# Kernel optimization log

Measured on AMD Instinct MI355X. Metric: run time of the kernel, lower is better.

Reference implementation:

```python
import jax, jax.numpy as jnp
import numpy as np

MARGIN = 0.3
EPS = 1e-12


def setup_inputs() -> dict:
    key = jax.random.key(0)
    k1, k2, k3 = jax.random.split(key, 3)
    B, D = 8192, 1024
    features = jax.random.normal(k1, (B, D), dtype=jnp.float32)
    labels = jax.random.randint(k2, (B,), 0, 100, dtype=jnp.int64)
    domain_labels = jax.random.randint(k3, (B,), 0, 2, dtype=jnp.int64)
    return {"features": features, "labels": labels, "domain_labels": domain_labels}


def reference(features, labels, domain_labels):
    # L2-normalize rows (F.normalize: x / max(||x||, eps))
    norm = jnp.maximum(jnp.linalg.norm(features, axis=1, keepdims=True), EPS)
    f = features / norm

    herb = domain_labels == 0   # [B] anchors
    field = domain_labels == 1  # [B] candidates

    sq = jnp.sum(f * f, axis=1)                                   # [B]
    d2 = sq[:, None] + sq[None, :] - 2.0 * jnp.einsum('id,jd->ij', f, f)
    d = jnp.sqrt(jnp.maximum(d2, 0.0))                            # [B, B]

    same = labels[:, None] == labels[None, :]                     # [B, B]
    pair = herb[:, None] & field[None, :]
    pos_mask = pair & same
    neg_mask = pair & ~same

    INF = jnp.float32(jnp.inf)
    pos_min = jnp.min(jnp.where(pos_mask, d, INF), axis=1)        # [B]
    neg_min = jnp.min(jnp.where(neg_mask, d, INF), axis=1)        # [B]

    valid = herb & jnp.any(pos_mask, axis=1) & jnp.any(neg_mask, axis=1)
    # Substitute 0 for invalid rows BEFORE subtracting to avoid inf - inf.
    pos_s = jnp.where(valid, pos_min, 0.0)
    neg_s = jnp.where(valid, neg_min, 0.0)
    tl = jnp.maximum(pos_s - neg_s + MARGIN, 0.0)                 # [B]

    loss_sum = jnp.sum(jnp.where(valid, tl, 0.0))
    count = jnp.sum(valid.astype(jnp.float32))
    return jnp.where(count > 0, loss_sum / jnp.maximum(count, 1.0), 0.0)
```

## Files before the change

### kernel.cpp

```cpp
#include <hip/hip_runtime.h>


#define B_ROWS 8192
#define DIM    1024

typedef __bf16 bf16x8 __attribute__((ext_vector_type(8)));
typedef float  f32x4  __attribute__((ext_vector_type(4)));

__device__ __forceinline__ unsigned short f2bf_rne(float x) {
    unsigned u = __float_as_uint(x);
    unsigned r = (u + 0x7FFFu + ((u >> 16) & 1u)) >> 16;
    return (unsigned short)r;
}
__device__ __forceinline__ float bf2f(unsigned short h) {
    return __uint_as_float(((unsigned)h) << 16);
}

__device__ __forceinline__ void async_copy16(const void* g, void* l) {
    __builtin_amdgcn_global_load_lds(
        (const __attribute__((address_space(1))) unsigned int*)g,
        (__attribute__((address_space(3))) unsigned int*)l,
        16, 0, 0);
}

__global__ __launch_bounds__(256) void compute_slots(
    const int* __restrict__ dom, int* __restrict__ slotOf,
    unsigned* __restrict__ cnt, float* __restrict__ accum)
{
    __shared__ int cnts[256];
    __shared__ int base[257];
    const int t = threadIdx.x;

    if (t == 0) {
        cnt[1] = 0u;
        accum[0] = 0.0f;
        accum[1] = 0.0f;
    }

    unsigned mask = 0u; int c = 0;
    #pragma unroll
    for (int i = 0; i < 32; ++i) {
        const int isA = (dom[t + 256 * i] == 0) ? 1 : 0;
        mask |= ((unsigned)isA) << i;
        c += isA;
    }
    cnts[t] = c;
    __syncthreads();
    if (t < 64) {
        const int c0 = cnts[4 * t + 0], c1 = cnts[4 * t + 1];
        const int c2 = cnts[4 * t + 2], c3 = cnts[4 * t + 3];
        const int s4 = c0 + c1 + c2 + c3;
        int sc = s4;
        #pragma unroll
        for (int d = 1; d < 64; d <<= 1) {
            const int o = __shfl_up(sc, d);
            if (t >= d) sc += o;
        }
        const int b = sc - s4;
        base[4 * t + 0] = b;
        base[4 * t + 1] = b + c0;
        base[4 * t + 2] = b + c0 + c1;
        base[4 * t + 3] = b + c0 + c1 + c2;
        if (t == 63) { base[256] = sc; cnt[0] = (unsigned)sc; }
    }
    __syncthreads();
    int aB = base[t];
    int fI = t * 32 - base[t];
    #pragma unroll
    for (int i = 0; i < 32; ++i) {
        const int isA = (mask >> i) & 1;
        slotOf[t + 256 * i] = isA ? aB : (8191 - fI);
        aB += isA;
        fI += 1 - isA;
    }
}

__global__ __launch_bounds__(256) void normalize_rows(
    const float* __restrict__ feat, const int* __restrict__ labels,
    int* slotOf , unsigned* __restrict__ negmin,
    unsigned short* __restrict__ G, int* __restrict__ labG,
    float* __restrict__ sqG)
{
    const int wv = threadIdx.x >> 6, lane = threadIdx.x & 63;
    const int row = blockIdx.x * 4 + wv;

    const float4* src = (const float4*)(feat + (size_t)row * DIM);
    float4 v[4];
    float ss = 0.0f;
    #pragma unroll
    for (int j = 0; j < 4; ++j) {
        v[j] = src[j * 64 + lane];
        ss += v[j].x * v[j].x + v[j].y * v[j].y + v[j].z * v[j].z + v[j].w * v[j].w;
    }
    #pragma unroll
    for (int s = 32; s > 0; s >>= 1) ss += __shfl_xor(ss, s);
    const float inv = 1.0f / fmaxf(sqrtf(ss), 1e-12f);

    const int slot = slotOf[row];
    if (lane == 0) {
        ((unsigned*)slotOf)[row] = 0xFFFFFFFFu;
        negmin[row] = 0xFFFFFFFFu;
    }
    unsigned short ub[16];
    float ss2 = 0.0f;
    #pragma unroll
    for (int j = 0; j < 4; ++j) {
        const float f0 = v[j].x * inv, f1 = v[j].y * inv,
                    f2 = v[j].z * inv, f3 = v[j].w * inv;
        ub[j * 4 + 0] = f2bf_rne(f0); ub[j * 4 + 1] = f2bf_rne(f1);
        ub[j * 4 + 2] = f2bf_rne(f2); ub[j * 4 + 3] = f2bf_rne(f3);
        #pragma unroll
        for (int q = 0; q < 4; ++q) {
            const float fr = bf2f(ub[j * 4 + q]);
            ss2 += fr * fr;
        }
    }
    #pragma unroll
    for (int s = 32; s > 0; s >>= 1) ss2 += __shfl_xor(ss2, s);
    if (lane == 0) {
        sqG[slot]  = ss2;
        labG[slot] = labels[row];
    }
    char* Gb = (char*)G;
    char* rowBase = Gb + (size_t)(slot >> 7) * 262144 + (size_t)(slot & 127) * 64
                       + (lane & 7) * 8;
    const int kc0 = lane >> 3;
    #pragma unroll
    for (int j = 0; j < 4; ++j) {
        ushort4 pk;
        pk.x = ub[j * 4 + 0]; pk.y = ub[j * 4 + 1];
        pk.z = ub[j * 4 + 2]; pk.w = ub[j * 4 + 3];
        *(ushort4*)(rowBase + (size_t)(j * 8 + kc0) * 8192) = pk;
    }
}

__global__ __launch_bounds__(256) void tile_mindist(
    const unsigned short* __restrict__ G, const int* __restrict__ labG,
    const float* __restrict__ sqG, const unsigned* __restrict__ cnt,
    unsigned* __restrict__ posmin, unsigned* __restrict__ negmin)
{
    const int nA = (int)cnt[0];
    const int nF = B_ROWS - nA;
    const int nTA = (nA + 127) >> 7;
    const int nTF = (nF + 127) >> 7;

    __shared__ __align__(16) unsigned short S[2][2][128 * 32];

    const int t = threadIdx.x;
    const int lane = t & 63, w = t >> 6;
    const int wm = w >> 1, wn = w & 1;
    const int l15 = lane & 15, quad = lane >> 4;

    const int ch0 = 2 * w;

    const int rdA  = (wm * 64 + l15) * 32 + quad * 8;
    const int rdF0 = ((1 - wn) * 64 + 15 - l15) * 32 + quad * 8;

    const char* Gb = (const char*)G;

    const int xcd = blockIdx.x & 7;
    const int bx  = xcd & 1;
    const int by  = xcd >> 1;
    const int qa = nTA >> 1, ra = nTA & 1;
    const int sa = qa + ((bx < ra) ? 1 : 0);
    const int xa = bx * qa + ((bx < ra) ? bx : ra);
    const int qf = nTF >> 2, rf = nTF & 3;
    const int sf = qf + ((by < rf) ? 1 : 0);
    const int ya = by * qf + ((by < rf) ? by : rf);
    const int localN = sa * sf;
    const int j0 = blockIdx.x >> 3;
    const int jstride = (int)(gridDim.x >> 3);

    for (int j = j0; j < localN; j += jstride) {
        const int tx = xa + j / sf;
        const int ty = ya + j % sf;
        const int rowA0  = tx * 128;
        const int rowFl0 = ty * 128;

        const char* baseA = Gb + (size_t)tx * 262144 + (size_t)(ch0 * 1024) + lane * 16;
        const char* baseF = Gb + (size_t)(63 - ty) * 262144 + (size_t)(ch0 * 1024) + lane * 16;

        f32x4 acc[4][4] = {};

        #pragma unroll
        for (int h = 0; h < 2; ++h) {
            async_copy16(baseA + h * 1024, &S[0][0][(ch0 + h) * 512]);
            async_copy16(baseF + h * 1024, &S[0][1][(ch0 + h) * 512]);
        }
        __syncthreads();

        #pragma unroll 4
        for (int step = 0; step < 32; ++step) {
            const int cur = step & 1;
            const int nb = cur ^ 1;
            if (step < 31) {
                const size_t off = (size_t)(step + 1) * 8192;
                #pragma unroll
                for (int h = 0; h < 2; ++h) {
                    async_copy16(baseA + off + h * 1024, &S[nb][0][(ch0 + h) * 512]);
                    async_copy16(baseF + off + h * 1024, &S[nb][1][(ch0 + h) * 512]);
                }
            }

            const unsigned short* pa = &S[cur][0][rdA];
            const unsigned short* pf = &S[cur][1][rdF0];
            bf16x8 a[4], b[4];
            #pragma unroll
            for (int fm = 0; fm < 4; ++fm) a[fm] = *(const bf16x8*)(pa + fm * 512);
            #pragma unroll
            for (int fn = 0; fn < 4; ++fn) b[fn] = *(const bf16x8*)(pf + (3 - fn) * 512);
            #pragma unroll
            for (int fm = 0; fm < 4; ++fm)
                #pragma unroll
                for (int fn = 0; fn < 4; ++fn)
                    acc[fm][fn] = __builtin_amdgcn_mfma_f32_16x16x32_bf16(
                        a[fm], b[fn], acc[fm][fn], 0, 0, 0);

            __syncthreads();
        }

        const float INFV = __uint_as_float(0x7f800000u);
        float sqf[4]; int lf_[4]; bool vf[4];
        #pragma unroll
        for (int fn = 0; fn < 4; ++fn) {
            const int rfl = rowFl0 + wn * 64 + fn * 16 + l15;
            vf[fn] = rfl < nF;
            const int slotF = 8191 - rfl;
            sqf[fn] = sqG[slotF];
            lf_[fn] = labG[slotF];
        }
        #pragma unroll
        for (int fm = 0; fm < 4; ++fm) {
            #pragma unroll
            for (int r = 0; r < 4; ++r) {
                const int ra2 = rowA0 + wm * 64 + fm * 16 + quad * 4 + r;
                const bool va = ra2 < nA;
                const int rac = va ? ra2 : 0;
                const float sqa = sqG[rac];
                const int la_ = labG[rac];
                float pmin = INFV, nmin = INFV;
                #pragma unroll
                for (int fn = 0; fn < 4; ++fn) {
                    const float dd = fmaxf(sqa + sqf[fn] - 2.0f * acc[fm][fn][r], 0.0f);
                    if (vf[fn]) {
                        if (la_ == lf_[fn]) pmin = fminf(pmin, dd);
                        else                nmin = fminf(nmin, dd);
                    }
                }
                #pragma unroll
                for (int s = 1; s < 16; s <<= 1) {
                    pmin = fminf(pmin, __shfl_xor(pmin, s));
                    nmin = fminf(nmin, __shfl_xor(nmin, s));
                }
                if (l15 == 0 && va) {
                    if (pmin < INFV) atomicMin(&posmin[ra2], __float_as_uint(pmin));
                    if (nmin < INFV) atomicMin(&negmin[ra2], __float_as_uint(nmin));
                }
            }
        }
        __syncthreads();
    }
}

__global__ __launch_bounds__(256) void reduce_loss(
    const unsigned* __restrict__ posmin, const unsigned* __restrict__ negmin,
    float* __restrict__ accum, unsigned* __restrict__ cnt,
    float* __restrict__ out)
{
    const int i = blockIdx.x * 256 + threadIdx.x;
    const unsigned up = posmin[i], un = negmin[i];
    float tl = 0.0f, c = 0.0f;
    if (up != 0xFFFFFFFFu && un != 0xFFFFFFFFu) {
        const float pd = sqrtf(__uint_as_float(up));
        const float nd = sqrtf(__uint_as_float(un));
        tl = fmaxf(pd - nd + 0.3f, 0.0f);
        c = 1.0f;
    }
    #pragma unroll
    for (int s = 32; s > 0; s >>= 1) {
        tl += __shfl_down(tl, s);
        c  += __shfl_down(c, s);
    }
    __shared__ float sb[8];
    const int lane = threadIdx.x & 63, w = threadIdx.x >> 6;
    if (lane == 0) { sb[w] = tl; sb[4 + w] = c; }
    __syncthreads();
    if (threadIdx.x == 0) {
        atomicAdd(&accum[0], sb[0] + sb[1] + sb[2] + sb[3]);
        atomicAdd(&accum[1], sb[4] + sb[5] + sb[6] + sb[7]);
        __threadfence();
        const unsigned ticket = atomicAdd(&cnt[1], 1u);
        if (ticket == 31u) {
            __threadfence();
            const float s2 = atomicAdd(&accum[0], 0.0f);
            const float c2 = atomicAdd(&accum[1], 0.0f);
            out[0] = (c2 > 0.0f) ? s2 / fmaxf(c2, 1.0f) : 0.0f;
        }
    }
}

extern "C" void kernel_launch(void* const* d_in, const int* in_sizes, int n_in,
                              void* d_out, int out_size, void* d_ws, size_t ws_size,
                              hipStream_t stream) {
    const float* feat  = (const float*)d_in[0];
    const int* labels  = (const int*)d_in[1];
    const int* dom     = (const int*)d_in[2];
    float* out = (float*)d_out;

    char* ws = (char*)d_ws;
    unsigned short* G   = (unsigned short*)(ws);
    int*      labG      = (int*)(ws + 16777216);
    float*    sqG       = (float*)(ws + 16809984);
    unsigned* posmin    = (unsigned*)(ws + 16842752);
    unsigned* negmin    = (unsigned*)(ws + 16875520);
    unsigned* cnt       = (unsigned*)(ws + 16908288);
    float*    accum     = (float*)(ws + 16908296);
    int*      slotOf    = (int*)(ws + 16842752);

    compute_slots<<<1, 256, 0, stream>>>(dom, slotOf, cnt, accum);
    normalize_rows<<<B_ROWS / 4, 256, 0, stream>>>(feat, labels, slotOf,
                                                   negmin, G, labG, sqG);

    tile_mindist<<<1056, 256, 0, stream>>>(G, labG, sqG, cnt, posmin, negmin);

    reduce_loss<<<B_ROWS / 256, 256, 0, stream>>>(posmin, negmin, accum, cnt, out);
}
```

Measured before the change: 165.5 us.

## Fuse slot computation into normalize and reduction into tile kernel via atomics

Removes the single-block compute_slots kernel by assigning slots through per-block atomic counters packed into one word (anchors low, candidates high), and removes the reduce_loss kernel by having the last-finishing tile_mindist block do the final reduction. A memset replaces the counter initialisation, and launch bounds on tile_mindist gain an occupancy hint. This cuts two launches and a serial one-block prefix scan, at the cost of a tail reduction done by one block and nondeterministic slot ordering.

```diff
diff --git a/kernel.cpp b/kernel.cpp
--- a/kernel.cpp
+++ b/kernel.cpp
@@ -23,123 +23,101 @@
         16, 0, 0);
 }
 
-__global__ __launch_bounds__(256) void compute_slots(
-    const int* __restrict__ dom, int* __restrict__ slotOf,
-    unsigned* __restrict__ cnt, float* __restrict__ accum)
-{
-    __shared__ int cnts[256];
-    __shared__ int base[257];
-    const int t = threadIdx.x;
-
-    if (t == 0) {
-        cnt[1] = 0u;
-        accum[0] = 0.0f;
-        accum[1] = 0.0f;
-    }
-
-    unsigned mask = 0u; int c = 0;
-    #pragma unroll
-    for (int i = 0; i < 32; ++i) {
-        const int isA = (dom[t + 256 * i] == 0) ? 1 : 0;
-        mask |= ((unsigned)isA) << i;
-        c += isA;
-    }
-    cnts[t] = c;
-    __syncthreads();
-    if (t < 64) {
-        const int c0 = cnts[4 * t + 0], c1 = cnts[4 * t + 1];
-        const int c2 = cnts[4 * t + 2], c3 = cnts[4 * t + 3];
-        const int s4 = c0 + c1 + c2 + c3;
-        int sc = s4;
-        #pragma unroll
-        for (int d = 1; d < 64; d <<= 1) {
-            const int o = __shfl_up(sc, d);
-            if (t >= d) sc += o;
-        }
-        const int b = sc - s4;
-        base[4 * t + 0] = b;
-        base[4 * t + 1] = b + c0;
-        base[4 * t + 2] = b + c0 + c1;
-        base[4 * t + 3] = b + c0 + c1 + c2;
-        if (t == 63) { base[256] = sc; cnt[0] = (unsigned)sc; }
-    }
-    __syncthreads();
-    int aB = base[t];
-    int fI = t * 32 - base[t];
-    #pragma unroll
-    for (int i = 0; i < 32; ++i) {
-        const int isA = (mask >> i) & 1;
-        slotOf[t + 256 * i] = isA ? aB : (8191 - fI);
-        aB += isA;
-        fI += 1 - isA;
-    }
-}
-
 __global__ __launch_bounds__(256) void normalize_rows(
     const float* __restrict__ feat, const int* __restrict__ labels,
-    int* slotOf , unsigned* __restrict__ negmin,
-    unsigned short* __restrict__ G, int* __restrict__ labG,
-    float* __restrict__ sqG)
+    const int* __restrict__ dom, unsigned* __restrict__ posmin,
+    unsigned* __restrict__ negmin, unsigned short* __restrict__ G,
+    int* __restrict__ labG, float* __restrict__ sqG,
+    unsigned* __restrict__ cnt)
 {
     const int wv = threadIdx.x >> 6, lane = threadIdx.x & 63;
-    const int row = blockIdx.x * 4 + wv;
-
-    const float4* src = (const float4*)(feat + (size_t)row * DIM);
-    float4 v[4];
-    float ss = 0.0f;
-    #pragma unroll
-    for (int j = 0; j < 4; ++j) {
-        v[j] = src[j * 64 + lane];
-        ss += v[j].x * v[j].x + v[j].y * v[j].y + v[j].z * v[j].z + v[j].w * v[j].w;
-    }
-    #pragma unroll
-    for (int s = 32; s > 0; s >>= 1) ss += __shfl_xor(ss, s);
-    const float inv = 1.0f / fmaxf(sqrtf(ss), 1e-12f);
-
-    const int slot = slotOf[row];
-    if (lane == 0) {
-        ((unsigned*)slotOf)[row] = 0xFFFFFFFFu;
-        negmin[row] = 0xFFFFFFFFu;
-    }
-    unsigned short ub[16];
-    float ss2 = 0.0f;
-    #pragma unroll
-    for (int j = 0; j < 4; ++j) {
-        const float f0 = v[j].x * inv, f1 = v[j].y * inv,
-                    f2 = v[j].z * inv, f3 = v[j].w * inv;
-        ub[j * 4 + 0] = f2bf_rne(f0); ub[j * 4 + 1] = f2bf_rne(f1);
-        ub[j * 4 + 2] = f2bf_rne(f2); ub[j * 4 + 3] = f2bf_rne(f3);
-        #pragma unroll
-        for (int q = 0; q < 4; ++q) {
-            const float fr = bf2f(ub[j * 4 + q]);
-            ss2 += fr * fr;
-        }
-    }
-    #pragma unroll
-    for (int s = 32; s > 0; s >>= 1) ss2 += __shfl_xor(ss2, s);
-    if (lane == 0) {
-        sqG[slot]  = ss2;
-        labG[slot] = labels[row];
-    }
+    const int r0 = blockIdx.x * 16;
+
+    __shared__ int enc[16];
+    __shared__ unsigned baseS;
+
+    if (threadIdx.x < 16)
+        enc[threadIdx.x] = (dom[r0 + threadIdx.x] == 0) ? 1 : 0;
+    __syncthreads();
+    if (threadIdx.x == 0) {
+        int na = 0;
+        #pragma unroll
+        for (int i = 0; i < 16; ++i) na += enc[i];
+        baseS = atomicAdd(cnt, (unsigned)na | ((unsigned)(16 - na) << 16));
+        int ra = 0, rf = 0;
+        #pragma unroll
+        for (int i = 0; i < 16; ++i) {
+            if (enc[i]) enc[i] = ra++;
+            else        enc[i] = 0x40000000 | rf++;
+        }
+    }
+    __syncthreads();
+    const unsigned baseA = baseS & 0xFFFFu;
+    const unsigned baseF = baseS >> 16;
+
     char* Gb = (char*)G;
-    char* rowBase = Gb + (size_t)(slot >> 7) * 262144 + (size_t)(slot & 127) * 64
-                       + (lane & 7) * 8;
-    const int kc0 = lane >> 3;
-    #pragma unroll
-    for (int j = 0; j < 4; ++j) {
-        ushort4 pk;
-        pk.x = ub[j * 4 + 0]; pk.y = ub[j * 4 + 1];
-        pk.z = ub[j * 4 + 2]; pk.w = ub[j * 4 + 3];
-        *(ushort4*)(rowBase + (size_t)(j * 8 + kc0) * 8192) = pk;
-    }
-}
-
-__global__ __launch_bounds__(256) void tile_mindist(
+    for (int k = 0; k < 4; ++k) {
+        const int li  = wv * 4 + k;
+        const int row = r0 + li;
+        const int e   = enc[li];
+        const int slot = (e & 0x40000000)
+                       ? (8191 - (int)(baseF + (e & 0xFFFF)))
+                       : (int)(baseA + e);
+
+        const float4* src = (const float4*)(feat + (size_t)row * DIM);
+        float4 v[4];
+        float ss = 0.0f;
+        #pragma unroll
+        for (int j = 0; j < 4; ++j) {
+            v[j] = src[j * 64 + lane];
+            ss += v[j].x * v[j].x + v[j].y * v[j].y + v[j].z * v[j].z + v[j].w * v[j].w;
+        }
+        #pragma unroll
+        for (int s = 32; s > 0; s >>= 1) ss += __shfl_xor(ss, s);
+        const float inv = 1.0f / fmaxf(sqrtf(ss), 1e-12f);
+
+        unsigned short ub[16];
+        float ss2 = 0.0f;
+        #pragma unroll
+        for (int j = 0; j < 4; ++j) {
+            const float f0 = v[j].x * inv, f1 = v[j].y * inv,
+                        f2 = v[j].z * inv, f3 = v[j].w * inv;
+            ub[j * 4 + 0] = f2bf_rne(f0); ub[j * 4 + 1] = f2bf_rne(f1);
+            ub[j * 4 + 2] = f2bf_rne(f2); ub[j * 4 + 3] = f2bf_rne(f3);
+            #pragma unroll
+            for (int q = 0; q < 4; ++q) {
+                const float fr = bf2f(ub[j * 4 + q]);
+                ss2 += fr * fr;
+            }
+        }
+        #pragma unroll
+        for (int s = 32; s > 0; s >>= 1) ss2 += __shfl_xor(ss2, s);
+        if (lane == 0) {
+            posmin[row] = 0xFFFFFFFFu;
+            negmin[row] = 0xFFFFFFFFu;
+            sqG[slot]  = ss2;
+            labG[slot] = labels[row];
+        }
+        char* rowBase = Gb + (size_t)(slot >> 7) * 262144
+                           + (size_t)(slot & 127) * 64 + (lane & 7) * 8;
+        const int kc0 = lane >> 3;
+        #pragma unroll
+        for (int j = 0; j < 4; ++j) {
+            ushort4 pk;
+            pk.x = ub[j * 4 + 0]; pk.y = ub[j * 4 + 1];
+            pk.z = ub[j * 4 + 2]; pk.w = ub[j * 4 + 3];
+            *(ushort4*)(rowBase + (size_t)(j * 8 + kc0) * 8192) = pk;
+        }
+    }
+}
+
+__global__ __launch_bounds__(256, 5) void tile_mindist(
     const unsigned short* __restrict__ G, const int* __restrict__ labG,
-    const float* __restrict__ sqG, const unsigned* __restrict__ cnt,
-    unsigned* __restrict__ posmin, unsigned* __restrict__ negmin)
+    const float* __restrict__ sqG, unsigned* __restrict__ cnt,
+    unsigned* __restrict__ posmin, unsigned* __restrict__ negmin,
+    float* __restrict__ out)
 {
-    const int nA = (int)cnt[0];
+    const int nA = (int)(cnt[0] & 0xFFFFu);
     const int nF = B_ROWS - nA;
     const int nTA = (nA + 127) >> 7;
     const int nTF = (nF + 127) >> 7;
@@ -260,40 +238,37 @@
         }
         __syncthreads();
     }
-}
-
-__global__ __launch_bounds__(256) void reduce_loss(
-    const unsigned* __restrict__ posmin, const unsigned* __restrict__ negmin,
-    float* __restrict__ accum, unsigned* __restrict__ cnt,
-    float* __restrict__ out)
-{
-    const int i = blockIdx.x * 256 + threadIdx.x;
-    const unsigned up = posmin[i], un = negmin[i];
-    float tl = 0.0f, c = 0.0f;
-    if (up != 0xFFFFFFFFu && un != 0xFFFFFFFFu) {
-        const float pd = sqrtf(__uint_as_float(up));
-        const float nd = sqrtf(__uint_as_float(un));
-        tl = fmaxf(pd - nd + 0.3f, 0.0f);
-        c = 1.0f;
-    }
-    #pragma unroll
-    for (int s = 32; s > 0; s >>= 1) {
-        tl += __shfl_down(tl, s);
-        c  += __shfl_down(c, s);
-    }
-    __shared__ float sb[8];
-    const int lane = threadIdx.x & 63, w = threadIdx.x >> 6;
-    if (lane == 0) { sb[w] = tl; sb[4 + w] = c; }
+
+    unsigned* flagp = (unsigned*)&S[1][1][0];
+    if (threadIdx.x == 0) {
+        __threadfence();
+        flagp[0] = (atomicAdd(&cnt[1], 1u) == (unsigned)(gridDim.x - 1)) ? 1u : 0u;
+    }
     __syncthreads();
-    if (threadIdx.x == 0) {
-        atomicAdd(&accum[0], sb[0] + sb[1] + sb[2] + sb[3]);
-        atomicAdd(&accum[1], sb[4] + sb[5] + sb[6] + sb[7]);
+    if (flagp[0]) {
         __threadfence();
-        const unsigned ticket = atomicAdd(&cnt[1], 1u);
-        if (ticket == 31u) {
-            __threadfence();
-            const float s2 = atomicAdd(&accum[0], 0.0f);
-            const float c2 = atomicAdd(&accum[1], 0.0f);
+        float tl = 0.0f, c = 0.0f;
+        for (int i = threadIdx.x; i < B_ROWS; i += 256) {
+            const unsigned up = atomicMin(&posmin[i], 0xFFFFFFFFu);
+            const unsigned un = atomicMin(&negmin[i], 0xFFFFFFFFu);
+            if (up != 0xFFFFFFFFu && un != 0xFFFFFFFFu) {
+                const float pd = sqrtf(__uint_as_float(up));
+                const float nd = sqrtf(__uint_as_float(un));
+                tl += fmaxf(pd - nd + 0.3f, 0.0f);
+                c  += 1.0f;
+            }
+        }
+        #pragma unroll
+        for (int s = 32; s > 0; s >>= 1) {
+            tl += __shfl_down(tl, s);
+            c  += __shfl_down(c, s);
+        }
+        float* sb = (float*)&S[0][0][0];
+        if (lane == 0) { sb[w] = tl; sb[4 + w] = c; }
+        __syncthreads();
+        if (threadIdx.x == 0) {
+            const float s2 = sb[0] + sb[1] + sb[2] + sb[3];
+            const float c2 = sb[4] + sb[5] + sb[6] + sb[7];
             out[0] = (c2 > 0.0f) ? s2 / fmaxf(c2, 1.0f) : 0.0f;
         }
     }
@@ -314,14 +289,13 @@
     unsigned* posmin    = (unsigned*)(ws + 16842752);
     unsigned* negmin    = (unsigned*)(ws + 16875520);
     unsigned* cnt       = (unsigned*)(ws + 16908288);
-    float*    accum     = (float*)(ws + 16908296);
-    int*      slotOf    = (int*)(ws + 16842752);
-
-    compute_slots<<<1, 256, 0, stream>>>(dom, slotOf, cnt, accum);
-    normalize_rows<<<B_ROWS / 4, 256, 0, stream>>>(feat, labels, slotOf,
-                                                   negmin, G, labG, sqG);
-
-    tile_mindist<<<1056, 256, 0, stream>>>(G, labG, sqG, cnt, posmin, negmin);
-
-    reduce_loss<<<B_ROWS / 256, 256, 0, stream>>>(posmin, negmin, accum, cnt, out);
-}
+
+    hipMemsetAsync(cnt, 0, 8, stream);
+
+    normalize_rows<<<B_ROWS / 16, 256, 0, stream>>>(feat, labels, dom,
+                                                    posmin, negmin, G, labG,
+                                                    sqG, cnt);
+
+    tile_mindist<<<1056, 256, 0, stream>>>(G, labG, sqG, cnt,
+                                           posmin, negmin, out);
+}
```

After: 238.1 us. 1.44x slower.

## Enlarge distance tile to 256x128 with 512-thread blocks

Applied to the files above, without the earlier changes.

Grows each workgroup's output tile from 128x128 to 256 anchor rows by 128 candidate rows, using 8 waves per block instead of 4. The candidate tile is shared across twice as many anchor rows, which lowers global and LDS traffic per MFMA. The shared-memory layout is flattened to hold 16 A chunks plus 8 F chunks per stage, and the grid shrinks to 512 blocks. The trade-offs are more LDS per block and fewer blocks in flight, which could hurt load balance or occupancy.

```diff
diff --git a/kernel.cpp b/kernel.cpp
--- a/kernel.cpp
+++ b/kernel.cpp
@@ -134,27 +134,26 @@
     }
 }
 
-__global__ __launch_bounds__(256) void tile_mindist(
+__global__ __launch_bounds__(512) void tile_mindist(
     const unsigned short* __restrict__ G, const int* __restrict__ labG,
     const float* __restrict__ sqG, const unsigned* __restrict__ cnt,
     unsigned* __restrict__ posmin, unsigned* __restrict__ negmin)
 {
     const int nA = (int)cnt[0];
     const int nF = B_ROWS - nA;
-    const int nTA = (nA + 127) >> 7;
+    const int nTA = (nA + 255) >> 8;
     const int nTF = (nF + 127) >> 7;
 
-    __shared__ __align__(16) unsigned short S[2][2][128 * 32];
+    __shared__ __align__(16) unsigned short S[2][384 * 32];
+    #define SF_OFF 8192
 
     const int t = threadIdx.x;
     const int lane = t & 63, w = t >> 6;
     const int wm = w >> 1, wn = w & 1;
     const int l15 = lane & 15, quad = lane >> 4;
 
-    const int ch0 = 2 * w;
-
     const int rdA  = (wm * 64 + l15) * 32 + quad * 8;
-    const int rdF0 = ((1 - wn) * 64 + 15 - l15) * 32 + quad * 8;
+    const int rdF0 = SF_OFF + ((1 - wn) * 64 + 15 - l15) * 32 + quad * 8;
 
     const char* Gb = (const char*)G;
 
@@ -174,19 +173,23 @@
     for (int j = j0; j < localN; j += jstride) {
         const int tx = xa + j / sf;
         const int ty = ya + j % sf;
-        const int rowA0  = tx * 128;
+        const int rowA0  = tx * 256;
         const int rowFl0 = ty * 128;
-
-        const char* baseA = Gb + (size_t)tx * 262144 + (size_t)(ch0 * 1024) + lane * 16;
-        const char* baseF = Gb + (size_t)(63 - ty) * 262144 + (size_t)(ch0 * 1024) + lane * 16;
+        const int pA0 = 2 * tx;
+
+        const int c0 = 2 * w;
+        const char* gA0 = Gb + (size_t)(pA0 + (c0 >> 3)) * 262144
+                             + (size_t)(c0 & 7) * 1024 + lane * 16;
+        const char* gA1 = Gb + (size_t)(pA0 + ((c0 + 1) >> 3)) * 262144
+                             + (size_t)((c0 + 1) & 7) * 1024 + lane * 16;
+        const char* gF  = Gb + (size_t)(63 - ty) * 262144
+                             + (size_t)w * 1024 + lane * 16;
 
         f32x4 acc[4][4] = {};
 
-        #pragma unroll
-        for (int h = 0; h < 2; ++h) {
-            async_copy16(baseA + h * 1024, &S[0][0][(ch0 + h) * 512]);
-            async_copy16(baseF + h * 1024, &S[0][1][(ch0 + h) * 512]);
-        }
+        async_copy16(gA0, &S[0][c0 * 512]);
+        async_copy16(gA1, &S[0][(c0 + 1) * 512]);
+        async_copy16(gF,  &S[0][SF_OFF + w * 512]);
         __syncthreads();
 
         #pragma unroll 4
@@ -195,15 +198,13 @@
             const int nb = cur ^ 1;
             if (step < 31) {
                 const size_t off = (size_t)(step + 1) * 8192;
-                #pragma unroll
-                for (int h = 0; h < 2; ++h) {
-                    async_copy16(baseA + off + h * 1024, &S[nb][0][(ch0 + h) * 512]);
-                    async_copy16(baseF + off + h * 1024, &S[nb][1][(ch0 + h) * 512]);
-                }
+                async_copy16(gA0 + off, &S[nb][c0 * 512]);
+                async_copy16(gA1 + off, &S[nb][(c0 + 1) * 512]);
+                async_copy16(gF + off,  &S[nb][SF_OFF + w * 512]);
             }
 
-            const unsigned short* pa = &S[cur][0][rdA];
-            const unsigned short* pf = &S[cur][1][rdF0];
+            const unsigned short* pa = &S[cur][rdA];
+            const unsigned short* pf = &S[cur][rdF0];
             bf16x8 a[4], b[4];
             #pragma unroll
             for (int fm = 0; fm < 4; ++fm) a[fm] = *(const bf16x8*)(pa + fm * 512);
@@ -260,6 +261,7 @@
         }
         __syncthreads();
     }
+    #undef SF_OFF
 }
 
 __global__ __launch_bounds__(256) void reduce_loss(
@@ -321,7 +323,7 @@
     normalize_rows<<<B_ROWS / 4, 256, 0, stream>>>(feat, labels, slotOf,
                                                    negmin, G, labG, sqG);
 
-    tile_mindist<<<1056, 256, 0, stream>>>(G, labG, sqG, cnt, posmin, negmin);
+    tile_mindist<<<512, 512, 0, stream>>>(G, labG, sqG, cnt, posmin, negmin);
 
     reduce_loss<<<B_ROWS / 256, 256, 0, stream>>>(posmin, negmin, accum, cnt, out);
 }
```

Measured after the change: 173.5 us. 1.05x slower.
